# Kernel tuning notes

Hardware: AMD Instinct MI355X
Metric: run time of the kernel (lower is better)

The kernel has to match this reference:

```python
import jax, jax.numpy as jnp
import numpy as np

B, S, HN, TN = 8, 32, 64, 512
HID, EMB, VOCAB = 512, 512, 10000


def setup_inputs():
    key = jax.random.key(0)
    k = jax.random.split(key, 14)
    w = lambda kk, shape: jax.random.normal(kk, shape, jnp.float32) * 0.02
    return {
        "dec_out": jax.random.normal(k[0], (B, S, HID), jnp.float32),
        "history": jax.random.normal(k[1], (B, HID), jnp.float32),
        "head": jax.random.randint(k[2], (B, HN), 0, VOCAB),
        "tail": jax.random.randint(k[3], (B, TN), 0, VOCAB),
        "adj_mask": jax.random.randint(k[4], (B, HN, TN), 0, 2).astype(bool),
        "dup_mask": jax.random.randint(k[5], (B, S, TN), 0, 2).astype(bool),
        "emb_table": w(k[6], (VOCAB, EMB)),
        "W_tq": w(k[7], (2 * HID + EMB, HID)),
        "b_tq": jnp.zeros((HID,), jnp.float32),
        "W_tk": w(k[8], (EMB, HID)),
        "b_tk": jnp.zeros((HID,), jnp.float32),
        "W_tout": w(k[9], (2 * HID, HID)),
        "W_hq": w(k[10], (2 * HID, HID)),
        "b_hq": jnp.zeros((HID,), jnp.float32),
        "W_hk": w(k[11], (HID, HID)),
        "b_hk": jnp.zeros((HID,), jnp.float32),
    }


def reference(dec_out, history, head, tail, adj_mask, dup_mask, emb_table,
              W_tq, b_tq, W_tk, b_tk, W_tout, W_hq, b_hq, W_hk, b_hk):
    head_emb = emb_table[head]  # (B, HN, EMB)
    tail_emb = emb_table[tail]  # (B, TN, EMB)

    # --- tail attention query: Linear(cat([dec_out, history, head_emb])) + ELU.
    # Same math as the torch broadcast-concat, computed as a sum of three
    # partial matmuls to avoid materializing the (B,S,HN,2*hid+emb) concat.
    Wd, Wh, We = W_tq[:HID], W_tq[HID:2 * HID], W_tq[2 * HID:]
    tq = jax.nn.elu((dec_out @ Wd)[:, :, None, :]
                    + (history @ Wh)[:, None, None, :]
                    + (head_emb @ We)[:, None, :, :]
                    + b_tq)                       # (B, S, HN, HID)
    tq = tq.reshape(B, S * HN, HID)
    tk = jax.nn.elu(tail_emb @ W_tk + b_tk)       # (B, TN, HID)  (dropout=eval)

    # combined logical mask: allowed = adjacency AND not-duplicate
    mask = (adj_mask[:, None, :, :] & ~dup_mask[:, :, None, :]).reshape(B, S * HN, TN)

    # GlobalAttention (dot): score -> mask -> softmax -> context -> tanh(linear_out([c;q]))
    scores = jnp.einsum('bqh,bth->bqt', tq, tk)   # (B, S*HN, TN)
    tail_attn = jax.nn.softmax(jnp.where(mask, scores, -jnp.inf), axis=-1)
    ctx = jnp.einsum('bqt,bth->bqh', tail_attn, tk)
    graph_hid = jnp.tanh(ctx @ W_tout[:HID] + tq @ W_tout[HID:])
    graph_hid = graph_hid.reshape(B * S, HN, HID)
    tail_attn = tail_attn.reshape(B * S, HN, TN)

    # --- head attention (one-step), length-masked over HN
    hq = jax.nn.elu(dec_out @ W_hq[:HID] + (history @ W_hq[HID:])[:, None, :] + b_hq)
    hq = hq.reshape(B * S, HID)
    hk = jax.nn.elu(jnp.einsum('nkh,hd->nkd', graph_hid, W_hk) + b_hk)
    lengths = jnp.repeat(jnp.sum(head != 0, axis=-1), S)          # (B*S,)
    hscores = jnp.einsum('nh,nkh->nk', hq, hk)                    # (B*S, HN)
    lmask = jnp.arange(HN)[None, :] < lengths[:, None]
    head_attn = jax.nn.softmax(jnp.where(lmask, hscores, -jnp.inf), axis=-1)
    # (head-attention context output is discarded by the original module)

    prob = jnp.einsum('nk,nkt->nt', head_attn, tail_attn).reshape(B, S, TN)
    return jnp.log(prob + 1e-20)
```

## Files before the change

### kernel.cpp

```cpp
#include <hip/hip_runtime.h>
#include <math.h>

#define BB 8
#define SS 32
#define HN 64
#define TN 512
#define HID 512

typedef __attribute__((ext_vector_type(8))) short short8;
typedef __attribute__((ext_vector_type(4))) float f32x4;

__device__ __forceinline__ float eluf(float x) { return x > 0.f ? x : (expf(x) - 1.f); }

__device__ __forceinline__ short f2bs(float f) {
    union { float f; unsigned int u; } v; v.f = f;
    unsigned int r = v.u + 0x7fffu + ((v.u >> 16) & 1u);
    return (short)(r >> 16);
}
__device__ __forceinline__ float b2f(short s) {
    union { unsigned int u; float f; } v;
    v.u = ((unsigned int)(unsigned short)s) << 16;
    return v.f;
}

__device__ __forceinline__ void gld16(const void* g, void* l) {
    __builtin_amdgcn_global_load_lds(
        (const __attribute__((address_space(1))) void*)g,
        (__attribute__((address_space(3))) void*)l, 16, 0, 0);
}

template <int ACT, int OUTB, int DUAL>
__device__ __forceinline__ void gcore(
    const short* __restrict__ A, const short* __restrict__ B,
    const short* __restrict__ A2, const short* __restrict__ B2,
    const float* __restrict__ bias, void* __restrict__ Cv,
    int ldc, int K, int m0, int n0, int cm0, short* Ls,
    const float* __restrict__ hq, float* __restrict__ hsp)
{
    short* Al = Ls;
    short* Bl = Ls + 8192;
    const int tid  = threadIdx.x;
    const int lane = tid & 63;
    const int w    = tid >> 6;
    const int wr   = w >> 1, wc = w & 1;
    const int l16  = lane & 15, quad = lane >> 4;

    const int srow = w * 16 + (lane >> 2);
    const int scol = (lane & 3) * 8;

    f32x4 acc[4][4];
#pragma unroll
    for (int i = 0; i < 4; ++i)
#pragma unroll
        for (int j = 0; j < 4; ++j) { acc[i][j][0]=0.f; acc[i][j][1]=0.f; acc[i][j][2]=0.f; acc[i][j][3]=0.f; }

    short* lA = Al + w * 512;
    short* lB = Bl + w * 512;
    const long rstep = (long)64 * K;

    for (int rep = 0; rep <= DUAL; ++rep) {
        const short* Ag = (rep ? A2 : A) + (long)(m0 + srow) * K + scol;
        const short* Bg = (rep ? B2 : B) + (long)(n0 + srow) * K + scol;
        for (int kt = 0; kt < K; kt += 64) {
            __syncthreads();
            gld16(Ag + kt, lA);
            gld16(Ag + kt + rstep, lA + 2048);
            gld16(Ag + kt + 32, lA + 4096);
            gld16(Ag + kt + 32 + rstep, lA + 4096 + 2048);
            gld16(Bg + kt, lB);
            gld16(Bg + kt + rstep, lB + 2048);
            gld16(Bg + kt + 32, lB + 4096);
            gld16(Bg + kt + 32 + rstep, lB + 4096 + 2048);
            __syncthreads();
#pragma unroll
            for (int h = 0; h < 2; ++h) {
                short8 af[4], bf4[4];
#pragma unroll
                for (int mi = 0; mi < 4; ++mi)
                    af[mi] = *(const short8*)(Al + h * 4096 + (wr * 64 + mi * 16 + l16) * 32 + quad * 8);
#pragma unroll
                for (int ni = 0; ni < 4; ++ni)
                    bf4[ni] = *(const short8*)(Bl + h * 4096 + (wc * 64 + ni * 16 + l16) * 32 + quad * 8);
#pragma unroll
                for (int mi = 0; mi < 4; ++mi)
#pragma unroll
                    for (int ni = 0; ni < 4; ++ni)
                        acc[mi][ni] = __builtin_amdgcn_mfma_f32_16x16x32_bf16(af[mi], bf4[ni], acc[mi][ni], 0, 0, 0);
            }
        }
    }

    __syncthreads();

    float bv[4];
#pragma unroll
    for (int ni = 0; ni < 4; ++ni)
        bv[ni] = bias ? bias[n0 + wc * 64 + ni * 16 + l16] : 0.f;

    if (OUTB == 1) {
        short* eb = Ls + w * 1152;
        const int er = lane >> 2;
        const int ec = (lane & 3) * 16;
#pragma unroll
        for (int mi = 0; mi < 4; ++mi) {
#pragma unroll
            for (int ni = 0; ni < 4; ++ni)
#pragma unroll
                for (int r = 0; r < 4; ++r) {
                    float x = acc[mi][ni][r] + bv[ni];
                    if (ACT == 1) x = eluf(x);
                    else if (ACT == 2) x = tanhf(x);
                    eb[(quad * 4 + r) * 72 + ni * 16 + l16] = f2bs(x);
                }
            __builtin_amdgcn_sched_barrier(0);
            short8 v0 = *(const short8*)&eb[er * 72 + ec];
            short8 v1 = *(const short8*)&eb[er * 72 + ec + 8];
            long cb = (long)(cm0 + wr * 64 + mi * 16 + er) * ldc + n0 + wc * 64 + ec;
            *(short8*)((short*)Cv + cb)     = v0;
            *(short8*)((short*)Cv + cb + 8) = v1;
            __builtin_amdgcn_sched_barrier(0);
        }
    } else if (OUTB == 2) {
        const int n_w = (cm0 + wr * 64) >> 6;
        float hqv[4];
#pragma unroll
        for (int ni = 0; ni < 4; ++ni)
            hqv[ni] = hq[(long)n_w * 512 + n0 + wc * 64 + ni * 16 + l16];
        float* red = (float*)Ls;
#pragma unroll
        for (int mi = 0; mi < 4; ++mi)
#pragma unroll
            for (int r = 0; r < 4; ++r) {
                float p = 0.f;
#pragma unroll
                for (int ni = 0; ni < 4; ++ni) {
                    float x = acc[mi][ni][r] + bv[ni];
                    if (ACT == 1) x = eluf(x);
                    p += x * hqv[ni];
                }
                p += __shfl_xor(p, 1);
                p += __shfl_xor(p, 2);
                p += __shfl_xor(p, 4);
                p += __shfl_xor(p, 8);
                if (l16 == 0) red[w * 64 + mi * 16 + quad * 4 + r] = p;
            }
        __syncthreads();
        if (tid < 128) {
            int wr2 = tid >> 6, rw = tid & 63;
            float v = red[(wr2 * 2 + 0) * 64 + rw] + red[(wr2 * 2 + 1) * 64 + rw];
            hsp[(long)(n0 >> 7) * 16384 + cm0 + tid] = v;
        }
    } else {
#pragma unroll
        for (int mi = 0; mi < 4; ++mi)
#pragma unroll
            for (int ni = 0; ni < 4; ++ni) {
                int gc = n0 + wc * 64 + ni * 16 + l16;
#pragma unroll
                for (int r = 0; r < 4; ++r) {
                    float x = acc[mi][ni][r] + bv[ni];
                    if (ACT == 1) x = eluf(x);
                    else if (ACT == 2) x = tanhf(x);
                    ((float*)Cv)[(long)(cm0 + wr * 64 + mi * 16 + quad * 4 + r) * ldc + gc] = x;
                }
            }
    }
}

template <int ACT, int OUTB, int DUAL, int NYL2>
__global__ __launch_bounds__(256) void mgemm_sw(
    const short* __restrict__ A, long sAz,
    const short* __restrict__ B, long sBz,
    const short* __restrict__ A2, long sA2z,
    const short* __restrict__ B2,
    const float* __restrict__ bias,
    void* __restrict__ Cv, long sCz, int ldc, int K)
{
    __shared__ short Ls[16384];
    const int bid = blockIdx.x;
    const int g = (bid & 7) + 8 * (bid >> 5);
    const int x = (bid >> 3) & 3;
    const int y = g & ((1 << NYL2) - 1);
    const int z = g >> NYL2;
    void* C = OUTB ? (void*)((short*)Cv + (long)z * sCz) : (void*)((float*)Cv + (long)z * sCz);
    const short* A2z = DUAL ? (A2 + (long)z * sA2z) : nullptr;
    gcore<ACT, OUTB, DUAL>(A + (long)z * sAz, B + (long)z * sBz, A2z, B2, bias, C,
                           ldc, K, y * 128, x * 128, y * 128, Ls, nullptr, nullptr);
}

__global__ __launch_bounds__(256) void mgemm_hs(
    const short* __restrict__ A, const short* __restrict__ B,
    const float* __restrict__ bias, const float* __restrict__ hq, float* __restrict__ hsp)
{
    __shared__ short Ls[16384];
    const int bid = blockIdx.x;
    const int y = (bid & 7) + 8 * (bid >> 5);
    const int x = (bid >> 3) & 3;
    gcore<1, 2, 0>(A, B, nullptr, nullptr, bias, nullptr, 512, 512,
                   y * 128, x * 128, y * 128, Ls, hq, hsp);
}

__global__ __launch_bounds__(256) void mgemm_multi(
    const short* __restrict__ decb, const short* __restrict__ WTall, float* __restrict__ qall,
    const short* __restrict__ embAll, const short* __restrict__ WTe, float* __restrict__ qe,
    const short* __restrict__ WTk, const float* __restrict__ b_tk, short* __restrict__ tkb)
{
    __shared__ short Ls[16384];
    int id = blockIdx.x;
    if (id < 48) {
        int y = id >> 4, x = id & 15;
        gcore<0, 0, 0>(decb, WTall, nullptr, nullptr, nullptr, qall, 2048, 512,
                       y * 128, x * 128, y * 128, Ls, nullptr, nullptr);
    } else if (id < 64) {
        int id2 = id - 48, y = id2 >> 2, x = id2 & 3;
        gcore<0, 0, 0>(embAll, WTe, nullptr, nullptr, nullptr, qe, 512, 512,
                       y * 128, x * 128, y * 128, Ls, nullptr, nullptr);
    } else {
        int id3 = id - 64, y = id3 >> 2, x = id3 & 3;
        gcore<1, 1, 0>(embAll, WTk, nullptr, nullptr, b_tk, tkb, 512, 512,
                       512 + y * 128, x * 128, y * 128, Ls, nullptr, nullptr);
    }
}

struct WTDesc { const float* src[9]; short* dst[9]; };

__global__ __launch_bounds__(256) void prep(
    const float* __restrict__ dec_out, const float* __restrict__ history,
    short* __restrict__ decb,
    const float* __restrict__ emb, const int* __restrict__ head, const int* __restrict__ tail,
    short* __restrict__ embAll, WTDesc wd)
{
    __shared__ float t[32][33];
    const int id = blockIdx.x, tid = threadIdx.x;
    if (id < 132) {
        int i = (id * 256 + tid) * 4;
        float4 v = (i < 131072) ? *(const float4*)(dec_out + i)
                                : *(const float4*)(history + (i - 131072));
        short4 o;
        o.x = f2bs(v.x); o.y = f2bs(v.y); o.z = f2bs(v.z); o.w = f2bs(v.w);
        *(short4*)(decb + i) = o;
    } else if (id < 132 + 2304) {
        int r = (id - 132) * 2 + (tid >> 7);
        int c4 = (tid & 127) * 4;
        int idx = (r < 512) ? head[r] : tail[r - 512];
        float4 v = *(const float4*)(emb + (long)idx * 512 + c4);
        short4 o;
        o.x = f2bs(v.x); o.y = f2bs(v.y); o.z = f2bs(v.z); o.w = f2bs(v.w);
        *(short4*)(embAll + (long)r * 512 + c4) = o;
    } else {
        int q = id - 2436;
        int z = q >> 8, xy = q & 255;
        int x = xy & 15, y = xy >> 4;
        const float* src = wd.src[z];
        short* dst = wd.dst[z];
        int k0 = y * 32, n0 = x * 32;
        int tx = tid & 31, ty = tid >> 5;
#pragma unroll
        for (int i = 0; i < 32; i += 8)
            t[ty + i][tx] = src[(long)(k0 + ty + i) * 512 + n0 + tx];
        __syncthreads();
#pragma unroll
        for (int i = 0; i < 32; i += 8)
            dst[(long)(n0 + ty + i) * 512 + k0 + tx] = f2bs(t[tx][ty + i]);
    }
}

__global__ __launch_bounds__(256) void l3_kernel(
    const float* __restrict__ qall, const float* __restrict__ qe,
    const float* __restrict__ b_tq, short* __restrict__ tqb,
    const short* __restrict__ WTo1, const short* __restrict__ tkb, short* __restrict__ tkWTb,
    const float* __restrict__ b_hq, float* __restrict__ hqf)
{
    __shared__ short Ls[16384];
    if (blockIdx.x < 8192) {
        long gid = (long)blockIdx.x * 256 + threadIdx.x;
        int r = (int)(gid >> 7), j0 = ((int)gid & 127) * 4;
        int b = r >> 11, rem = r & 2047, s = rem >> 6, h = rem & 63;
        float4 d = *(const float4*)(qall + (long)(b * 32 + s) * 2048 + j0);
        float4 q = *(const float4*)(qall + (long)(256 + b) * 2048 + 1024 + j0);
        float4 e = *(const float4*)(qe + (long)(b * 64 + h) * 512 + j0);
        float4 bb = *(const float4*)(b_tq + j0);
        short4 o;
        o.x = f2bs(eluf(d.x + q.x + e.x + bb.x));
        o.y = f2bs(eluf(d.y + q.y + e.y + bb.y));
        o.z = f2bs(eluf(d.z + q.z + e.z + bb.z));
        o.w = f2bs(eluf(d.w + q.w + e.w + bb.w));
        *(short4*)(tqb + (long)r * 512 + j0) = o;
    } else if (blockIdx.x < 8320) {
        int id2 = blockIdx.x - 8192;
        int z = id2 >> 4, r = id2 & 15;
        int x = r & 3, y = r >> 2;
        gcore<0, 1, 0>(WTo1, tkb + (long)z * 262144, nullptr, nullptr, nullptr,
                       tkWTb + (long)z * 262144, 512, 512, y * 128, x * 128, y * 128, Ls,
                       nullptr, nullptr);
    } else {
        long gid = (long)(blockIdx.x - 8320) * 256 + threadIdx.x;
        int n = (int)(gid >> 7), j0 = ((int)gid & 127) * 4;
        int b = n >> 5;
        float4 d = *(const float4*)(qall + (long)n * 2048 + 512 + j0);
        float4 h2 = *(const float4*)(qall + (long)(256 + b) * 2048 + 1536 + j0);
        float4 bb = *(const float4*)(b_hq + j0);
        float4 o;
        o.x = eluf(d.x + h2.x + bb.x);
        o.y = eluf(d.y + h2.y + bb.y);
        o.z = eluf(d.z + h2.z + bb.z);
        o.w = eluf(d.w + h2.w + bb.w);
        *(float4*)(hqf + (long)n * 512 + j0) = o;
    }
}

__global__ __launch_bounds__(256) void sm_kernel(
    const short* __restrict__ sc, const int* __restrict__ adj, const int* __restrict__ dup,
    short* __restrict__ Pb)
{
    int w = threadIdx.x >> 6, lane = threadIdx.x & 63;
    long r = (long)blockIdx.x * 4 + w;
    int b = (int)(r >> 11), rem = (int)(r & 2047), s = rem >> 6, h = rem & 63;
    const short* row = sc + r * 512 + lane * 8;
    const int* adjr = adj + ((long)(b * 64 + h)) * 512 + lane * 8;
    const int* dupr = dup + ((long)(b * 32 + s)) * 512 + lane * 8;
    short8 v8 = *(const short8*)row;
    int4 a0 = *(const int4*)adjr, a1 = *(const int4*)(adjr + 4);
    int4 d0 = *(const int4*)dupr, d1 = *(const int4*)(dupr + 4);
    int am[8] = {a0.x, a0.y, a0.z, a0.w, a1.x, a1.y, a1.z, a1.w};
    int dm[8] = {d0.x, d0.y, d0.z, d0.w, d1.x, d1.y, d1.z, d1.w};
    float v[8];
    float m = -INFINITY;
#pragma unroll
    for (int i = 0; i < 8; ++i) {
        v[i] = (am[i] && !dm[i]) ? b2f(v8[i]) : -INFINITY;
        m = fmaxf(m, v[i]);
    }
#pragma unroll
    for (int d = 32; d >= 1; d >>= 1) m = fmaxf(m, __shfl_xor(m, d));
    float sum = 0.f;
#pragma unroll
    for (int i = 0; i < 8; ++i) {
        float e = (m == -INFINITY) ? 0.f : expf(v[i] - m);
        v[i] = e; sum += e;
    }
#pragma unroll
    for (int d = 32; d >= 1; d >>= 1) sum += __shfl_xor(sum, d);
    float inv = sum > 0.f ? 1.f / sum : 0.f;
    short8 o;
#pragma unroll
    for (int i = 0; i < 8; ++i) o[i] = f2bs(v[i] * inv);
    *(short8*)(Pb + r * 512 + lane * 8) = o;
}

__global__ __launch_bounds__(256) void fused_head(
    const float* __restrict__ hsp, const int* __restrict__ head,
    const short* __restrict__ ta, float* __restrict__ out)
{
    int n = blockIdx.x, b = n >> 5;
    int tid = threadIdx.x;
    __shared__ float hal[64];
    __shared__ float part[4][512];

    if (tid < 64) {
        float sv_raw = hsp[n * 64 + tid] + hsp[16384 + n * 64 + tid]
                     + hsp[2 * 16384 + n * 64 + tid] + hsp[3 * 16384 + n * 64 + tid];
        int hv = head[b * 64 + tid];
        unsigned long long ball = __ballot(hv != 0);
        int len = __popcll(ball);
        float sv = (tid < len) ? sv_raw : -INFINITY;
        float m = sv;
#pragma unroll
        for (int d = 32; d >= 1; d >>= 1) m = fmaxf(m, __shfl_xor(m, d));
        float e = expf(sv - m);
        float sum = e;
#pragma unroll
        for (int d = 32; d >= 1; d >>= 1) sum += __shfl_xor(sum, d);
        hal[tid] = e / sum;
    }
    __syncthreads();

    {
        int w = tid >> 6, lane = tid & 63;
        const short* tab = ta + (long)n * 64 * 512 + (long)(w * 16) * 512 + lane * 8;
        float acc[8] = {};
#pragma unroll
        for (int k = 0; k < 16; ++k) {
            float a = hal[w * 16 + k];
            short8 tv = *(const short8*)(tab + (long)k * 512);
#pragma unroll
            for (int u = 0; u < 8; ++u) acc[u] += a * b2f(tv[u]);
        }
        float4* pp = (float4*)&part[w][lane * 8];
        pp[0] = make_float4(acc[0], acc[1], acc[2], acc[3]);
        pp[1] = make_float4(acc[4], acc[5], acc[6], acc[7]);
    }
    __syncthreads();

    for (int t = tid; t < 512; t += 256) {
        float a = part[0][t] + part[1][t] + part[2][t] + part[3][t];
        out[(long)n * 512 + t] = logf(a + 1e-20f);
    }
}

extern "C" void kernel_launch(void* const* d_in, const int* in_sizes, int n_in,
                              void* d_out, int out_size, void* d_ws, size_t ws_size,
                              hipStream_t stream)
{
    const float* dec_out = (const float*)d_in[0];
    const float* history = (const float*)d_in[1];
    const int*   head    = (const int*)d_in[2];
    const int*   tail    = (const int*)d_in[3];
    const int*   adj     = (const int*)d_in[4];
    const int*   dup     = (const int*)d_in[5];
    const float* emb     = (const float*)d_in[6];
    const float* W_tq    = (const float*)d_in[7];
    const float* b_tq    = (const float*)d_in[8];
    const float* W_tk    = (const float*)d_in[9];
    const float* b_tk    = (const float*)d_in[10];
    const float* W_tout  = (const float*)d_in[11];
    const float* W_hq    = (const float*)d_in[12];
    const float* b_hq    = (const float*)d_in[13];
    const float* W_hk    = (const float*)d_in[14];
    const float* b_hk    = (const float*)d_in[15];
    float* out = (float*)d_out;

    char* ws = (char*)d_ws;
    auto alloc = [&](size_t bytes) -> void* {
        char* p = ws;
        ws += (bytes + 255) & ~(size_t)255;
        return (void*)p;
    };
    short* decb   = (short*)alloc((size_t)384 * 512 * 2);
    short* embAll = (short*)alloc((size_t)4608 * 512 * 2);
    short* WT     = (short*)alloc((size_t)9 * 512 * 512 * 2);
    float* qall   = (float*)alloc((size_t)384 * 2048 * 4);
    float* qe     = (float*)alloc((size_t)512 * 512 * 4);
    float* hqf    = (float*)alloc((size_t)256 * 512 * 4);
    float* hsp    = (float*)alloc((size_t)4 * 16384 * 4);
    short* tkb    = (short*)alloc((size_t)4096 * 512 * 2);
    short* tkWTb  = (short*)alloc((size_t)4096 * 512 * 2);
    short* tqb    = (short*)alloc((size_t)16384 * 512 * 2);
    short* scb    = (short*)alloc((size_t)16384 * 512 * 2);
    short* Pb     = (short*)alloc((size_t)16384 * 512 * 2);
    short* ghb = scb;

    WTDesc wd;
    wd.src[0] = W_tq;               wd.dst[0] = WT;
    wd.src[1] = W_hq;               wd.dst[1] = WT + (size_t)1 * 262144;
    wd.src[2] = W_tq + 512 * 512;   wd.dst[2] = WT + (size_t)2 * 262144;
    wd.src[3] = W_hq + 512 * 512;   wd.dst[3] = WT + (size_t)3 * 262144;
    wd.src[4] = W_tq + 1024 * 512;  wd.dst[4] = WT + (size_t)4 * 262144;
    wd.src[5] = W_tk;               wd.dst[5] = WT + (size_t)5 * 262144;
    wd.src[6] = W_tout;             wd.dst[6] = WT + (size_t)6 * 262144;
    wd.src[7] = W_tout + 512 * 512; wd.dst[7] = WT + (size_t)7 * 262144;
    wd.src[8] = W_hk;               wd.dst[8] = WT + (size_t)8 * 262144;

    prep<<<4740, 256, 0, stream>>>(dec_out, history, decb, emb, head, tail, embAll, wd);
    mgemm_multi<<<192, 256, 0, stream>>>(decb, WT, qall, embAll, WT + (size_t)4 * 262144, qe,
                                         WT + (size_t)5 * 262144, b_tk, tkb);
    l3_kernel<<<8448, 256, 0, stream>>>(qall, qe, b_tq, tqb, WT + (size_t)6 * 262144, tkb, tkWTb,
                                        b_hq, hqf);
    mgemm_sw<0, 1, 0, 4><<<512, 256, 0, stream>>>(
        tqb, (long)2048 * 512, tkb, 262144, nullptr, 0, nullptr, nullptr,
        scb, (long)2048 * 512, 512, 512);
    sm_kernel<<<4096, 256, 0, stream>>>(scb, adj, dup, Pb);
    mgemm_sw<2, 1, 1, 4><<<512, 256, 0, stream>>>(
        Pb, (long)2048 * 512, tkWTb, 262144, tqb, (long)2048 * 512, WT + (size_t)7 * 262144,
        nullptr, ghb, (long)2048 * 512, 512, 512);
    mgemm_hs<<<512, 256, 0, stream>>>(ghb, WT + (size_t)8 * 262144, b_hk, hqf, hsp);
    fused_head<<<256, 256, 0, stream>>>(hsp, head, Pb, out);
}
```

Baseline: 218.4 us.

## Fuse scores+softmax and graph_hid+head-attention into full-row per-query kernels

Replaces five launches (scores GEMM, softmax, dual GEMM for graph_hid, head-score GEMM, head combine) with two kernels. Each block owns one (b,s) group of 64 rows across the full 512 columns. The first computes scores and applies mask and softmax in registers. The second computes the tanh graph_hid tile into LDS, multiplies by W_hk, reduces against hq and finishes head softmax and the output log-prob. This removes intermediate bf16 score and graph_hid round-trips to global memory and several launches. In exchange each kernel runs only 256 blocks of 512 threads, which may underfill the GPU. It also uses large LDS and small 32-wide k-steps with no double buffering.

```diff
diff --git a/kernel.cpp b/kernel.cpp
--- a/kernel.cpp
+++ b/kernel.cpp
@@ -29,13 +29,11 @@
         (__attribute__((address_space(3))) void*)l, 16, 0, 0);
 }
 
-template <int ACT, int OUTB, int DUAL>
+template <int ACT, int OUTB>
 __device__ __forceinline__ void gcore(
     const short* __restrict__ A, const short* __restrict__ B,
-    const short* __restrict__ A2, const short* __restrict__ B2,
     const float* __restrict__ bias, void* __restrict__ Cv,
-    int ldc, int K, int m0, int n0, int cm0, short* Ls,
-    const float* __restrict__ hq, float* __restrict__ hsp)
+    int ldc, int K, int m0, int n0, int cm0, short* Ls)
 {
     short* Al = Ls;
     short* Bl = Ls + 8192;
@@ -58,35 +56,33 @@
     short* lB = Bl + w * 512;
     const long rstep = (long)64 * K;
 
-    for (int rep = 0; rep <= DUAL; ++rep) {
-        const short* Ag = (rep ? A2 : A) + (long)(m0 + srow) * K + scol;
-        const short* Bg = (rep ? B2 : B) + (long)(n0 + srow) * K + scol;
-        for (int kt = 0; kt < K; kt += 64) {
-            __syncthreads();
-            gld16(Ag + kt, lA);
-            gld16(Ag + kt + rstep, lA + 2048);
-            gld16(Ag + kt + 32, lA + 4096);
-            gld16(Ag + kt + 32 + rstep, lA + 4096 + 2048);
-            gld16(Bg + kt, lB);
-            gld16(Bg + kt + rstep, lB + 2048);
-            gld16(Bg + kt + 32, lB + 4096);
-            gld16(Bg + kt + 32 + rstep, lB + 4096 + 2048);
-            __syncthreads();
-#pragma unroll
-            for (int h = 0; h < 2; ++h) {
-                short8 af[4], bf4[4];
-#pragma unroll
-                for (int mi = 0; mi < 4; ++mi)
-                    af[mi] = *(const short8*)(Al + h * 4096 + (wr * 64 + mi * 16 + l16) * 32 + quad * 8);
+    const short* Ag = A + (long)(m0 + srow) * K + scol;
+    const short* Bg = B + (long)(n0 + srow) * K + scol;
+    for (int kt = 0; kt < K; kt += 64) {
+        __syncthreads();
+        gld16(Ag + kt, lA);
+        gld16(Ag + kt + rstep, lA + 2048);
+        gld16(Ag + kt + 32, lA + 4096);
+        gld16(Ag + kt + 32 + rstep, lA + 4096 + 2048);
+        gld16(Bg + kt, lB);
+        gld16(Bg + kt + rstep, lB + 2048);
+        gld16(Bg + kt + 32, lB + 4096);
+        gld16(Bg + kt + 32 + rstep, lB + 4096 + 2048);
+        __syncthreads();
+#pragma unroll
+        for (int h = 0; h < 2; ++h) {
+            short8 af[4], bf4[4];
+#pragma unroll
+            for (int mi = 0; mi < 4; ++mi)
+                af[mi] = *(const short8*)(Al + h * 4096 + (wr * 64 + mi * 16 + l16) * 32 + quad * 8);
+#pragma unroll
+            for (int ni = 0; ni < 4; ++ni)
+                bf4[ni] = *(const short8*)(Bl + h * 4096 + (wc * 64 + ni * 16 + l16) * 32 + quad * 8);
+#pragma unroll
+            for (int mi = 0; mi < 4; ++mi)
 #pragma unroll
                 for (int ni = 0; ni < 4; ++ni)
-                    bf4[ni] = *(const short8*)(Bl + h * 4096 + (wc * 64 + ni * 16 + l16) * 32 + quad * 8);
-#pragma unroll
-                for (int mi = 0; mi < 4; ++mi)
-#pragma unroll
-                    for (int ni = 0; ni < 4; ++ni)
-                        acc[mi][ni] = __builtin_amdgcn_mfma_f32_16x16x32_bf16(af[mi], bf4[ni], acc[mi][ni], 0, 0, 0);
-            }
+                    acc[mi][ni] = __builtin_amdgcn_mfma_f32_16x16x32_bf16(af[mi], bf4[ni], acc[mi][ni], 0, 0, 0);
         }
     }
 
@@ -109,7 +105,6 @@
                 for (int r = 0; r < 4; ++r) {
                     float x = acc[mi][ni][r] + bv[ni];
                     if (ACT == 1) x = eluf(x);
-                    else if (ACT == 2) x = tanhf(x);
                     eb[(quad * 4 + r) * 72 + ni * 16 + l16] = f2bs(x);
                 }
             __builtin_amdgcn_sched_barrier(0);
@@ -120,36 +115,6 @@
             *(short8*)((short*)Cv + cb + 8) = v1;
             __builtin_amdgcn_sched_barrier(0);
         }
-    } else if (OUTB == 2) {
-        const int n_w = (cm0 + wr * 64) >> 6;
-        float hqv[4];
-#pragma unroll
-        for (int ni = 0; ni < 4; ++ni)
-            hqv[ni] = hq[(long)n_w * 512 + n0 + wc * 64 + ni * 16 + l16];
-        float* red = (float*)Ls;
-#pragma unroll
-        for (int mi = 0; mi < 4; ++mi)
-#pragma unroll
-            for (int r = 0; r < 4; ++r) {
-                float p = 0.f;
-#pragma unroll
-                for (int ni = 0; ni < 4; ++ni) {
-                    float x = acc[mi][ni][r] + bv[ni];
-                    if (ACT == 1) x = eluf(x);
-                    p += x * hqv[ni];
-                }
-                p += __shfl_xor(p, 1);
-                p += __shfl_xor(p, 2);
-                p += __shfl_xor(p, 4);
-                p += __shfl_xor(p, 8);
-                if (l16 == 0) red[w * 64 + mi * 16 + quad * 4 + r] = p;
-            }
-        __syncthreads();
-        if (tid < 128) {
-            int wr2 = tid >> 6, rw = tid & 63;
-            float v = red[(wr2 * 2 + 0) * 64 + rw] + red[(wr2 * 2 + 1) * 64 + rw];
-            hsp[(long)(n0 >> 7) * 16384 + cm0 + tid] = v;
-        }
     } else {
 #pragma unroll
         for (int mi = 0; mi < 4; ++mi)
@@ -160,44 +125,10 @@
                 for (int r = 0; r < 4; ++r) {
                     float x = acc[mi][ni][r] + bv[ni];
                     if (ACT == 1) x = eluf(x);
-                    else if (ACT == 2) x = tanhf(x);
                     ((float*)Cv)[(long)(cm0 + wr * 64 + mi * 16 + quad * 4 + r) * ldc + gc] = x;
                 }
             }
     }
-}
-
-template <int ACT, int OUTB, int DUAL, int NYL2>
-__global__ __launch_bounds__(256) void mgemm_sw(
-    const short* __restrict__ A, long sAz,
-    const short* __restrict__ B, long sBz,
-    const short* __restrict__ A2, long sA2z,
-    const short* __restrict__ B2,
-    const float* __restrict__ bias,
-    void* __restrict__ Cv, long sCz, int ldc, int K)
-{
-    __shared__ short Ls[16384];
-    const int bid = blockIdx.x;
-    const int g = (bid & 7) + 8 * (bid >> 5);
-    const int x = (bid >> 3) & 3;
-    const int y = g & ((1 << NYL2) - 1);
-    const int z = g >> NYL2;
-    void* C = OUTB ? (void*)((short*)Cv + (long)z * sCz) : (void*)((float*)Cv + (long)z * sCz);
-    const short* A2z = DUAL ? (A2 + (long)z * sA2z) : nullptr;
-    gcore<ACT, OUTB, DUAL>(A + (long)z * sAz, B + (long)z * sBz, A2z, B2, bias, C,
-                           ldc, K, y * 128, x * 128, y * 128, Ls, nullptr, nullptr);
-}
-
-__global__ __launch_bounds__(256) void mgemm_hs(
-    const short* __restrict__ A, const short* __restrict__ B,
-    const float* __restrict__ bias, const float* __restrict__ hq, float* __restrict__ hsp)
-{
-    __shared__ short Ls[16384];
-    const int bid = blockIdx.x;
-    const int y = (bid & 7) + 8 * (bid >> 5);
-    const int x = (bid >> 3) & 3;
-    gcore<1, 2, 0>(A, B, nullptr, nullptr, bias, nullptr, 512, 512,
-                   y * 128, x * 128, y * 128, Ls, hq, hsp);
 }
 
 __global__ __launch_bounds__(256) void mgemm_multi(
@@ -209,16 +140,13 @@
     int id = blockIdx.x;
     if (id < 48) {
         int y = id >> 4, x = id & 15;
-        gcore<0, 0, 0>(decb, WTall, nullptr, nullptr, nullptr, qall, 2048, 512,
-                       y * 128, x * 128, y * 128, Ls, nullptr, nullptr);
+        gcore<0, 0>(decb, WTall, nullptr, qall, 2048, 512, y * 128, x * 128, y * 128, Ls);
     } else if (id < 64) {
         int id2 = id - 48, y = id2 >> 2, x = id2 & 3;
-        gcore<0, 0, 0>(embAll, WTe, nullptr, nullptr, nullptr, qe, 512, 512,
-                       y * 128, x * 128, y * 128, Ls, nullptr, nullptr);
+        gcore<0, 0>(embAll, WTe, nullptr, qe, 512, 512, y * 128, x * 128, y * 128, Ls);
     } else {
         int id3 = id - 64, y = id3 >> 2, x = id3 & 3;
-        gcore<1, 1, 0>(embAll, WTk, nullptr, nullptr, b_tk, tkb, 512, 512,
-                       512 + y * 128, x * 128, y * 128, Ls, nullptr, nullptr);
+        gcore<1, 1>(embAll, WTk, b_tk, tkb, 512, 512, 512 + y * 128, x * 128, y * 128, Ls);
     }
 }
 
@@ -290,9 +218,8 @@
         int id2 = blockIdx.x - 8192;
         int z = id2 >> 4, r = id2 & 15;
         int x = r & 3, y = r >> 2;
-        gcore<0, 1, 0>(WTo1, tkb + (long)z * 262144, nullptr, nullptr, nullptr,
-                       tkWTb + (long)z * 262144, 512, 512, y * 128, x * 128, y * 128, Ls,
-                       nullptr, nullptr);
+        gcore<0, 1>(WTo1, tkb + (long)z * 262144, nullptr,
+                    tkWTb + (long)z * 262144, 512, 512, y * 128, x * 128, y * 128, Ls);
     } else {
         long gid = (long)(blockIdx.x - 8320) * 256 + threadIdx.x;
         int n = (int)(gid >> 7), j0 = ((int)gid & 127) * 4;
@@ -309,61 +236,232 @@
     }
 }
 
-__global__ __launch_bounds__(256) void sm_kernel(
-    const short* __restrict__ sc, const int* __restrict__ adj, const int* __restrict__ dup,
-    short* __restrict__ Pb)
-{
-    int w = threadIdx.x >> 6, lane = threadIdx.x & 63;
-    long r = (long)blockIdx.x * 4 + w;
-    int b = (int)(r >> 11), rem = (int)(r & 2047), s = rem >> 6, h = rem & 63;
-    const short* row = sc + r * 512 + lane * 8;
-    const int* adjr = adj + ((long)(b * 64 + h)) * 512 + lane * 8;
-    const int* dupr = dup + ((long)(b * 32 + s)) * 512 + lane * 8;
-    short8 v8 = *(const short8*)row;
-    int4 a0 = *(const int4*)adjr, a1 = *(const int4*)(adjr + 4);
-    int4 d0 = *(const int4*)dupr, d1 = *(const int4*)(dupr + 4);
-    int am[8] = {a0.x, a0.y, a0.z, a0.w, a1.x, a1.y, a1.z, a1.w};
-    int dm[8] = {d0.x, d0.y, d0.z, d0.w, d1.x, d1.y, d1.z, d1.w};
-    float v[8];
-    float m = -INFINITY;
-#pragma unroll
-    for (int i = 0; i < 8; ++i) {
-        v[i] = (am[i] && !dm[i]) ? b2f(v8[i]) : -INFINITY;
-        m = fmaxf(m, v[i]);
-    }
-#pragma unroll
-    for (int d = 32; d >= 1; d >>= 1) m = fmaxf(m, __shfl_xor(m, d));
-    float sum = 0.f;
-#pragma unroll
-    for (int i = 0; i < 8; ++i) {
-        float e = (m == -INFINITY) ? 0.f : expf(v[i] - m);
-        v[i] = e; sum += e;
-    }
-#pragma unroll
-    for (int d = 32; d >= 1; d >>= 1) sum += __shfl_xor(sum, d);
-    float inv = sum > 0.f ? 1.f / sum : 0.f;
-    short8 o;
-#pragma unroll
-    for (int i = 0; i < 8; ++i) o[i] = f2bs(v[i] * inv);
-    *(short8*)(Pb + r * 512 + lane * 8) = o;
-}
-
-__global__ __launch_bounds__(256) void fused_head(
-    const float* __restrict__ hsp, const int* __restrict__ head,
-    const short* __restrict__ ta, float* __restrict__ out)
-{
-    int n = blockIdx.x, b = n >> 5;
-    int tid = threadIdx.x;
+__device__ __forceinline__ void gemm8_acc(
+    const short* __restrict__ Ag, const short* __restrict__ Bg,
+    short* AL, short* BL, f32x4 acc[4][4],
+    int w, int lane, int l16, int quad)
+{
+    const short* ap = Ag + ((w & 3) * 16 + (lane >> 2)) * 512 + (lane & 3) * 8;
+    const short* bp = Bg + (long)(w * 64 + (lane >> 2)) * 512 + (lane & 3) * 8;
+    for (int kt = 0; kt < 512; kt += 32) {
+        __syncthreads();
+        if (w < 4) gld16(ap + kt, AL + (w & 3) * 512);
+#pragma unroll
+        for (int u = 0; u < 4; ++u)
+            gld16(bp + (long)u * 16 * 512 + kt, BL + (w * 64 + u * 16) * 32);
+        __syncthreads();
+        short8 af[4], bf[4];
+#pragma unroll
+        for (int mi = 0; mi < 4; ++mi)
+            af[mi] = *(const short8*)(AL + (mi * 16 + l16) * 32 + quad * 8);
+#pragma unroll
+        for (int ni = 0; ni < 4; ++ni)
+            bf[ni] = *(const short8*)(BL + (w * 64 + ni * 16 + l16) * 32 + quad * 8);
+#pragma unroll
+        for (int mi = 0; mi < 4; ++mi)
+#pragma unroll
+            for (int ni = 0; ni < 4; ++ni)
+                acc[mi][ni] = __builtin_amdgcn_mfma_f32_16x16x32_bf16(af[mi], bf[ni], acc[mi][ni], 0, 0, 0);
+    }
+}
+
+__global__ __launch_bounds__(512) void k4_scores_sm(
+    const short* __restrict__ tqb, const short* __restrict__ tkb,
+    const int* __restrict__ adj, const int* __restrict__ dup, short* __restrict__ Pb)
+{
+    __shared__ short AL[2048];
+    __shared__ short BL[16384];
+    __shared__ float red[8][64];
+    __shared__ float rowv[64];
+    const int n = blockIdx.x, b = n >> 5;
+    const int tid = threadIdx.x, lane = tid & 63, w = tid >> 6;
+    const int l16 = lane & 15, quad = lane >> 4;
+
+    f32x4 acc[4][4];
+#pragma unroll
+    for (int i = 0; i < 4; ++i)
+#pragma unroll
+        for (int j = 0; j < 4; ++j) { acc[i][j][0]=0.f; acc[i][j][1]=0.f; acc[i][j][2]=0.f; acc[i][j][3]=0.f; }
+
+    gemm8_acc(tqb + (long)n * 64 * 512, tkb + (long)b * 262144, AL, BL, acc, w, lane, l16, quad);
+
+    const int* adjb = adj + (long)(b * 64) * 512;
+    const int* dupb = dup + (long)n * 512;
+#pragma unroll
+    for (int mi = 0; mi < 4; ++mi)
+#pragma unroll
+        for (int ni = 0; ni < 4; ++ni) {
+            int col = w * 64 + ni * 16 + l16;
+            int dv = dupb[col];
+#pragma unroll
+            for (int r = 0; r < 4; ++r) {
+                int row = mi * 16 + quad * 4 + r;
+                if (!(adjb[(long)row * 512 + col] && !dv)) acc[mi][ni][r] = -INFINITY;
+            }
+        }
+
+#pragma unroll
+    for (int mi = 0; mi < 4; ++mi)
+#pragma unroll
+        for (int r = 0; r < 4; ++r) {
+            float m = fmaxf(fmaxf(acc[mi][0][r], acc[mi][1][r]),
+                            fmaxf(acc[mi][2][r], acc[mi][3][r]));
+            m = fmaxf(m, __shfl_xor(m, 1));
+            m = fmaxf(m, __shfl_xor(m, 2));
+            m = fmaxf(m, __shfl_xor(m, 4));
+            m = fmaxf(m, __shfl_xor(m, 8));
+            if (l16 == 0) red[w][mi * 16 + quad * 4 + r] = m;
+        }
+    __syncthreads();
+    if (tid < 64) {
+        float m = red[0][tid];
+#pragma unroll
+        for (int ww = 1; ww < 8; ++ww) m = fmaxf(m, red[ww][tid]);
+        rowv[tid] = m;
+    }
+    __syncthreads();
+
+#pragma unroll
+    for (int mi = 0; mi < 4; ++mi)
+#pragma unroll
+        for (int r = 0; r < 4; ++r) {
+            int row = mi * 16 + quad * 4 + r;
+            float m = rowv[row];
+            float s = 0.f;
+#pragma unroll
+            for (int ni = 0; ni < 4; ++ni) {
+                float e = (m == -INFINITY) ? 0.f : expf(acc[mi][ni][r] - m);
+                acc[mi][ni][r] = e;
+                s += e;
+            }
+            s += __shfl_xor(s, 1);
+            s += __shfl_xor(s, 2);
+            s += __shfl_xor(s, 4);
+            s += __shfl_xor(s, 8);
+            if (l16 == 0) red[w][row] = s;
+        }
+    __syncthreads();
+    if (tid < 64) {
+        float s = 0.f;
+#pragma unroll
+        for (int ww = 0; ww < 8; ++ww) s += red[ww][tid];
+        rowv[tid] = s > 0.f ? 1.f / s : 0.f;
+    }
+    __syncthreads();
+
+    short* eb = BL + w * 1152;
+    const int er = lane >> 2, ec = (lane & 3) * 16;
+#pragma unroll
+    for (int mi = 0; mi < 4; ++mi) {
+#pragma unroll
+        for (int ni = 0; ni < 4; ++ni)
+#pragma unroll
+            for (int r = 0; r < 4; ++r) {
+                int row = mi * 16 + quad * 4 + r;
+                eb[(quad * 4 + r) * 72 + ni * 16 + l16] = f2bs(acc[mi][ni][r] * rowv[row]);
+            }
+        __builtin_amdgcn_sched_barrier(0);
+        short8 v0 = *(const short8*)&eb[er * 72 + ec];
+        short8 v1 = *(const short8*)&eb[er * 72 + ec + 8];
+        long cb = ((long)n * 64 + mi * 16 + er) * 512 + w * 64 + ec;
+        *(short8*)(Pb + cb)     = v0;
+        *(short8*)(Pb + cb + 8) = v1;
+        __builtin_amdgcn_sched_barrier(0);
+    }
+}
+
+__global__ __launch_bounds__(512) void k5_ghmega(
+    const short* __restrict__ Pb, const short* __restrict__ tqb,
+    const short* __restrict__ tkWTb, const short* __restrict__ WTo2,
+    const short* __restrict__ WThk, const float* __restrict__ b_hk,
+    const float* __restrict__ hqf, const int* __restrict__ head,
+    float* __restrict__ out)
+{
+    __shared__ short AL[2048];
+    __shared__ short BL[16384];
+    __shared__ short GH[64 * 520];
+    __shared__ float red[8][64];
     __shared__ float hal[64];
-    __shared__ float part[4][512];
+    const int n = blockIdx.x, b = n >> 5;
+    const int tid = threadIdx.x, lane = tid & 63, w = tid >> 6;
+    const int l16 = lane & 15, quad = lane >> 4;
+
+    f32x4 acc[4][4];
+#pragma unroll
+    for (int i = 0; i < 4; ++i)
+#pragma unroll
+        for (int j = 0; j < 4; ++j) { acc[i][j][0]=0.f; acc[i][j][1]=0.f; acc[i][j][2]=0.f; acc[i][j][3]=0.f; }
+
+    gemm8_acc(Pb + (long)n * 64 * 512, tkWTb + (long)b * 262144, AL, BL, acc, w, lane, l16, quad);
+    gemm8_acc(tqb + (long)n * 64 * 512, WTo2, AL, BL, acc, w, lane, l16, quad);
+
+#pragma unroll
+    for (int mi = 0; mi < 4; ++mi)
+#pragma unroll
+        for (int ni = 0; ni < 4; ++ni)
+#pragma unroll
+            for (int r = 0; r < 4; ++r)
+                GH[(mi * 16 + quad * 4 + r) * 520 + w * 64 + ni * 16 + l16] =
+                    f2bs(tanhf(acc[mi][ni][r]));
+    __syncthreads();
+
+#pragma unroll
+    for (int i = 0; i < 4; ++i)
+#pragma unroll
+        for (int j = 0; j < 4; ++j) { acc[i][j][0]=0.f; acc[i][j][1]=0.f; acc[i][j][2]=0.f; acc[i][j][3]=0.f; }
+    {
+        const short* bp = WThk + (long)(w * 64 + (lane >> 2)) * 512 + (lane & 3) * 8;
+        for (int kt = 0; kt < 512; kt += 32) {
+            __syncthreads();
+#pragma unroll
+            for (int u = 0; u < 4; ++u)
+                gld16(bp + (long)u * 16 * 512 + kt, BL + (w * 64 + u * 16) * 32);
+            __syncthreads();
+            short8 af[4], bf[4];
+#pragma unroll
+            for (int mi = 0; mi < 4; ++mi)
+                af[mi] = *(const short8*)(GH + (mi * 16 + l16) * 520 + kt + quad * 8);
+#pragma unroll
+            for (int ni = 0; ni < 4; ++ni)
+                bf[ni] = *(const short8*)(BL + (w * 64 + ni * 16 + l16) * 32 + quad * 8);
+#pragma unroll
+            for (int mi = 0; mi < 4; ++mi)
+#pragma unroll
+                for (int ni = 0; ni < 4; ++ni)
+                    acc[mi][ni] = __builtin_amdgcn_mfma_f32_16x16x32_bf16(af[mi], bf[ni], acc[mi][ni], 0, 0, 0);
+        }
+    }
+
+    float bv[4], hqv[4];
+#pragma unroll
+    for (int ni = 0; ni < 4; ++ni) {
+        int col = w * 64 + ni * 16 + l16;
+        bv[ni]  = b_hk[col];
+        hqv[ni] = hqf[(long)n * 512 + col];
+    }
+#pragma unroll
+    for (int mi = 0; mi < 4; ++mi)
+#pragma unroll
+        for (int r = 0; r < 4; ++r) {
+            float p = 0.f;
+#pragma unroll
+            for (int ni = 0; ni < 4; ++ni)
+                p += eluf(acc[mi][ni][r] + bv[ni]) * hqv[ni];
+            p += __shfl_xor(p, 1);
+            p += __shfl_xor(p, 2);
+            p += __shfl_xor(p, 4);
+            p += __shfl_xor(p, 8);
+            if (l16 == 0) red[w][mi * 16 + quad * 4 + r] = p;
+        }
+    __syncthreads();
 
     if (tid < 64) {
-        float sv_raw = hsp[n * 64 + tid] + hsp[16384 + n * 64 + tid]
-                     + hsp[2 * 16384 + n * 64 + tid] + hsp[3 * 16384 + n * 64 + tid];
+        float sv = red[0][tid] + red[1][tid] + red[2][tid] + red[3][tid]
+                 + red[4][tid] + red[5][tid] + red[6][tid] + red[7][tid];
         int hv = head[b * 64 + tid];
         unsigned long long ball = __ballot(hv != 0);
         int len = __popcll(ball);
-        float sv = (tid < len) ? sv_raw : -INFINITY;
+        sv = (tid < len) ? sv : -INFINITY;
         float m = sv;
 #pragma unroll
         for (int d = 32; d >= 1; d >>= 1) m = fmaxf(m, __shfl_xor(m, d));
@@ -375,26 +473,27 @@
     }
     __syncthreads();
 
+    float* part = (float*)BL;
     {
-        int w = tid >> 6, lane = tid & 63;
-        const short* tab = ta + (long)n * 64 * 512 + (long)(w * 16) * 512 + lane * 8;
-        float acc[8] = {};
-#pragma unroll
-        for (int k = 0; k < 16; ++k) {
-            float a = hal[w * 16 + k];
-            short8 tv = *(const short8*)(tab + (long)k * 512);
-#pragma unroll
-            for (int u = 0; u < 8; ++u) acc[u] += a * b2f(tv[u]);
-        }
-        float4* pp = (float4*)&part[w][lane * 8];
-        pp[0] = make_float4(acc[0], acc[1], acc[2], acc[3]);
-        pp[1] = make_float4(acc[4], acc[5], acc[6], acc[7]);
-    }
-    __syncthreads();
-
-    for (int t = tid; t < 512; t += 256) {
-        float a = part[0][t] + part[1][t] + part[2][t] + part[3][t];
-        out[(long)n * 512 + t] = logf(a + 1e-20f);
+        float pacc[8] = {};
+        const short* prow = Pb + ((long)n * 64 + w * 8) * 512 + lane * 8;
+#pragma unroll
+        for (int kk = 0; kk < 8; ++kk) {
+            float a = hal[w * 8 + kk];
+            short8 tv = *(const short8*)(prow + (long)kk * 512);
+#pragma unroll
+            for (int u = 0; u < 8; ++u) pacc[u] += a * b2f(tv[u]);
+        }
+        float4* pp = (float4*)&part[w * 512 + lane * 8];
+        pp[0] = make_float4(pacc[0], pacc[1], pacc[2], pacc[3]);
+        pp[1] = make_float4(pacc[4], pacc[5], pacc[6], pacc[7]);
+    }
+    __syncthreads();
+    {
+        float a = 0.f;
+#pragma unroll
+        for (int ww = 0; ww < 8; ++ww) a += part[ww * 512 + tid];
+        out[(long)n * 512 + tid] = logf(a + 1e-20f);
     }
 }
 
@@ -432,13 +531,10 @@
     float* qall   = (float*)alloc((size_t)384 * 2048 * 4);
     float* qe     = (float*)alloc((size_t)512 * 512 * 4);
     float* hqf    = (float*)alloc((size_t)256 * 512 * 4);
-    float* hsp    = (float*)alloc((size_t)4 * 16384 * 4);
     short* tkb    = (short*)alloc((size_t)4096 * 512 * 2);
     short* tkWTb  = (short*)alloc((size_t)4096 * 512 * 2);
     short* tqb    = (short*)alloc((size_t)16384 * 512 * 2);
-    short* scb    = (short*)alloc((size_t)16384 * 512 * 2);
     short* Pb     = (short*)alloc((size_t)16384 * 512 * 2);
-    short* ghb = scb;
 
     WTDesc wd;
     wd.src[0] = W_tq;               wd.dst[0] = WT;
@@ -456,13 +552,7 @@
                                          WT + (size_t)5 * 262144, b_tk, tkb);
     l3_kernel<<<8448, 256, 0, stream>>>(qall, qe, b_tq, tqb, WT + (size_t)6 * 262144, tkb, tkWTb,
                                         b_hq, hqf);
-    mgemm_sw<0, 1, 0, 4><<<512, 256, 0, stream>>>(
-        tqb, (long)2048 * 512, tkb, 262144, nullptr, 0, nullptr, nullptr,
-        scb, (long)2048 * 512, 512, 512);
-    sm_kernel<<<4096, 256, 0, stream>>>(scb, adj, dup, Pb);
-    mgemm_sw<2, 1, 1, 4><<<512, 256, 0, stream>>>(
-        Pb, (long)2048 * 512, tkWTb, 262144, tqb, (long)2048 * 512, WT + (size_t)7 * 262144,
-        nullptr, ghb, (long)2048 * 512, 512, 512);
-    mgemm_hs<<<512, 256, 0, stream>>>(ghb, WT + (size_t)8 * 262144, b_hk, hqf, hsp);
-    fused_head<<<256, 256, 0, stream>>>(hsp, head, Pb, out);
-}
+    k4_scores_sm<<<256, 512, 0, stream>>>(tqb, tkb, adj, dup, Pb);
+    k5_ghmega<<<256, 512, 0, stream>>>(Pb, tqb, tkWTb, WT + (size_t)7 * 262144,
+                                       WT + (size_t)8 * 262144, b_hk, hqf, head, out);
+}
```

Result: slower. 235.6 us (+7.9%).
